# Kernel optimization log

Hardware: AMD Instinct MI355X
Metric: run time of the kernel (lower is better)

## Reference

```python
import jax, jax.numpy as jnp
import numpy as np

B, N, C, H, W = 16, 8, 3, 64, 96
PRED_BITS = 2
CONV_CH, FC, FMAP_H, FMAP_W = 16, 100, 16, 24


def _conv(x, Wc, bc):
    # x: [n, cin, 64, 96] -> [n, 16, 16, 24]; kernel 8x8, stride 4, pad 2
    y = jax.lax.conv_general_dilated(x, Wc, (4, 4), [(2, 2), (2, 2)],
                                     dimension_numbers=('NCHW', 'OIHW', 'NCHW'))
    return y + bc[None, :, None, None]


def _encoder(x, Wc, bc, W2, b2, W3, b3):
    h1 = jax.nn.relu(_conv(x, Wc, bc)).reshape(x.shape[0], -1)  # [n, 6144]
    h2 = jax.nn.relu(h1 @ W2 + b2)
    return h2 @ W3 + b3  # [n, PRED_BITS]


def _gumbel_softmax(logits, g, temp):
    return jax.nn.softmax((logits + g) / temp, axis=-1)


def setup_inputs() -> dict:
    key = jax.random.key(0)
    ks = jax.random.split(key, 16)
    rn = lambda k, s, sc=1.0: jax.random.normal(k, s, jnp.float32) * sc
    gum = lambda k, s: -jnp.log(-jnp.log(jax.random.uniform(k, s, jnp.float32, 1e-6, 1.0 - 1e-6)))
    inp = {
        'state': rn(ks[0], (B, N, C, H, W)),
        'state_next': rn(ks[1], (B, N, C, H, W)),
        'state_tilda': rn(ks[2], (B, N, C, H, W)),
        'n_obj': jax.random.randint(ks[3], (B,), 1, N + 1),
        'temp': jnp.asarray(1.0, jnp.float32),
        'g_unary': gum(ks[4], (3, B * N, PRED_BITS)),
        'g_binary': gum(ks[5], (3, B * N * N, PRED_BITS)),
        'Wc_u': rn(ks[6], (CONV_CH, C, 8, 8), 0.05),
        'bc_u': jnp.zeros((CONV_CH,), jnp.float32),
        'W2_u': rn(ks[7], (CONV_CH * FMAP_H * FMAP_W, FC), 0.02),
        'b2_u': jnp.zeros((FC,), jnp.float32),
        'W3_u': rn(ks[8], (FC, PRED_BITS), 0.1),
        'b3_u': jnp.zeros((PRED_BITS,), jnp.float32),
        'Wc_b': rn(ks[9], (CONV_CH, 2 * C, 8, 8), 0.05),
        'bc_b': jnp.zeros((CONV_CH,), jnp.float32),
        'W2_b': rn(ks[10], (CONV_CH * FMAP_H * FMAP_W, FC), 0.02),
        'b2_b': jnp.zeros((FC,), jnp.float32),
        'W3_b': rn(ks[11], (FC, PRED_BITS), 0.1),
        'b3_b': jnp.zeros((PRED_BITS,), jnp.float32),
    }
    return inp


def reference(state, state_next, state_tilda, n_obj, temp, g_unary, g_binary,
              Wc_u, bc_u, W2_u, b2_u, W3_u, b3_u,
              Wc_b, bc_b, W2_b, b2_b, W3_b, b3_b):
    # cartesian-product pair gather (padded to N_max^2 per sample)
    ii = jnp.arange(N * N) // N
    jj = jnp.arange(N * N) % N

    def pairs(s):  # [B,N,C,H,W] -> [B*N*N, 2C, H, W]
        return jnp.concatenate([s[:, ii], s[:, jj]], axis=2).reshape(B * N * N, 2 * C, H, W)

    def bin_pred(s, g):
        logits = _encoder(pairs(s), Wc_b, bc_b, W2_b, b2_b, W3_b, b3_b)
        return _gumbel_softmax(logits, g, temp).reshape(B, N * N, PRED_BITS)

    def un_pred(s, g):
        logits = _encoder(s.reshape(B * N, C, H, W), Wc_u, bc_u, W2_u, b2_u, W3_u, b3_u)
        return _gumbel_softmax(logits, g, temp).reshape(B, N, PRED_BITS)

    bp = bin_pred(state, g_binary[0])
    bp_n = bin_pred(state_next, g_binary[1])
    bp_t = bin_pred(state_tilda, g_binary[2])
    up = un_pred(state, g_unary[0])
    up_n = un_pred(state_next, g_unary[1])
    up_t = un_pred(state_tilda, g_unary[2])

    # compact the valid n^2 pairs to the front (matches torch padded scatter layout)
    n = n_obj[:, None]                      # [B,1]
    p = jnp.arange(N * N)[None, :]          # [1,N^2]
    ns = jnp.maximum(n, 1)
    k = (p // ns) * N + (p % ns)            # padded index of compact position p
    valid_b = (p < n * n)[:, :, None]
    kidx = jnp.clip(k, 0, N * N - 1)[:, :, None]

    def compact(x):
        return jnp.take_along_axis(x, kidx, axis=1) * valid_b

    valid_u = (jnp.arange(N)[None, :] < n)[:, :, None]

    return (compact(bp), compact(bp_n), compact(bp_t),
            up * valid_u, up_n * valid_u, up_t * valid_u)
```

## Files before the change

### kernel.cpp

```cpp
#include <hip/hip_runtime.h>
#include <hip/hip_fp16.h>


typedef __attribute__((ext_vector_type(8))) _Float16 f16x8;
typedef __attribute__((ext_vector_type(4))) float f32x4;

__device__ inline unsigned short h16u(float x) {
    __half h = __float2half(x);
    return __builtin_bit_cast(unsigned short, h);
}

__device__ inline uint4 pair_relu4(uint4 f, uint4 s) {
    f16x8 a = __builtin_bit_cast(f16x8, f);
    f16x8 b = __builtin_bit_cast(f16x8, s);
    const f16x8 z = {0, 0, 0, 0, 0, 0, 0, 0};
    f16x8 r = a + b;
    r = __builtin_elementwise_max(r, z);
    return __builtin_bit_cast(uint4, r);
}

#define CL_STRIDE 106
#define CL_CH (36 * CL_STRIDE)
__global__ __launch_bounds__(256) void conv_prep_kernel(
    const float* __restrict__ s0, const float* __restrict__ s1, const float* __restrict__ s2,
    const float* __restrict__ Wcu, const float* __restrict__ Wcb,
    const float* __restrict__ bcu, const float* __restrict__ bcb,
    const float* __restrict__ W2b, const float* __restrict__ W2u,
    unsigned short* __restrict__ Au, unsigned short* __restrict__ yfb,
    unsigned short* __restrict__ ysb,
    unsigned short* __restrict__ Btb, unsigned short* __restrict__ Btu)
{
    __shared__ __align__(16) unsigned short sh[3 * CL_CH];
    const int bx  = blockIdx.x;
    const int tid = threadIdx.x;

    if (bx >= 768) {
        const int bx2 = bx - 768;
        const int arr = bx2 / 48;
        const int k0 = (bx2 % 48) * 128;
        const float* W2 = arr ? W2u : W2b;
        unsigned short* Bt = arr ? Btu : Btb;
#pragma unroll
        for (int p = 0; p < 2; ++p) {
            const int kk0 = p * 64;
            __syncthreads();
            for (int t = tid; t < 64 * 128; t += 256) {
                int kk = t >> 7, f = t & 127;
                float v = (f < 100) ? W2[(long)(k0 + kk0 + kk) * 100 + f] : 0.f;
                sh[kk * 130 + f] = h16u(v);
            }
            __syncthreads();
            for (int t = tid; t < 64 * 128; t += 256) {
                int f = t >> 6, kk = t & 63;
                Bt[(long)f * 6144 + k0 + kk0 + kk] = sh[kk * 130 + f];
            }
        }
        return;
    }

    const int si  = bx >> 8;
    const int rem = bx & 255;
    const int img = rem >> 1;
    const int h   = rem & 1;
    const float* simg = (si == 0 ? s0 : (si == 1 ? s1 : s2)) + (long)img * 18432;

    const int lane = tid & 63;
    const int w    = tid >> 6;
    const int quad = lane >> 4;
    const int lcol = lane & 15;

    {
        unsigned* d = (unsigned*)sh;
        const float4* Wu4 = (const float4*)Wcu;
        for (int l4 = tid; l4 < 768; l4 += 256) {
            int l = l4 * 4, ch = l / 192, e = l % 192;
            int g = (e >> 5) * 3;
            int bi = ((g * 64 + ((e >> 3) & 3) * 16 + ch) * 8 + (e & 7)) >> 1;
            float4 v = Wu4[l4];
            d[bi]     = (unsigned)h16u(v.x) | ((unsigned)h16u(v.y) << 16);
            d[bi + 1] = (unsigned)h16u(v.z) | ((unsigned)h16u(v.w) << 16);
        }
        const float4* Wb4 = (const float4*)Wcb;
        for (int l4 = tid; l4 < 1536; l4 += 256) {
            int l = l4 * 4, ch = l / 384, r = l % 384;
            int nt = (r < 192) ? 1 : 2, e = r % 192;
            int g = (e >> 5) * 3 + nt;
            int bi = ((g * 64 + ((e >> 3) & 3) * 16 + ch) * 8 + (e & 7)) >> 1;
            float4 v = Wb4[l4];
            d[bi]     = (unsigned)h16u(v.x) | ((unsigned)h16u(v.y) << 16);
            d[bi + 1] = (unsigned)h16u(v.z) | ((unsigned)h16u(v.w) << 16);
        }
    }
    __syncthreads();

    f16x8 bw[6][3];
#pragma unroll
    for (int t6 = 0; t6 < 6; ++t6)
#pragma unroll
        for (int nt = 0; nt < 3; ++nt)
            bw[t6][nt] = *(const f16x8*)(sh + ((t6 * 3 + nt) * 64 + lane) * 8);
    __syncthreads();

    for (int t = tid; t < (3 * CL_CH) / 2; t += 256)
        ((unsigned*)sh)[t] = 0u;
    __syncthreads();

    const int y0 = h * 32;
    for (int t = tid; t < 3 * 36 * 24; t += 256) {
        int c = t / 864, rq = t % 864, r = rq / 24, q = rq % 24;
        int iy = y0 + r - 2;
        if (iy >= 0 && iy < 64) {
            float4 v = *((const float4*)(simg + c * 6144 + iy * 96) + q);
            unsigned lo = (unsigned)h16u(v.x) | ((unsigned)h16u(v.y) << 16);
            unsigned hi = (unsigned)h16u(v.z) | ((unsigned)h16u(v.w) << 16);
            unsigned* dst = (unsigned*)(sh + c * CL_CH + r * CL_STRIDE + q * 4 + 4);
            dst[0] = lo; dst[1] = hi;
        }
    }
    __syncthreads();

    const float bu = bcu[lcol];
    const float bb = bcb[lcol];

    f32x4 accs[3][3];
#pragma unroll
    for (int mi = 0; mi < 3; ++mi)
#pragma unroll
        for (int nt = 0; nt < 3; ++nt) accs[mi][nt] = (f32x4){0.f, 0.f, 0.f, 0.f};

#pragma unroll
    for (int mi = 0; mi < 3; ++mi) {
        const int mt = w * 3 + mi;
        const int p  = mt * 16 + lcol;
        const int oyl = p / 24, ox = p % 24;
#pragma unroll
        for (int t6 = 0; t6 < 6; ++t6) {
            int g  = t6 * 4 + quad;
            int c  = g >> 3, ky = g & 7;
            const unsigned* lp = (const unsigned*)(sh + c * CL_CH + (oyl * 4 + ky) * CL_STRIDE + ox * 4 + 2);
            f16x8 afr;
            unsigned* ap = (unsigned*)&afr;
            ap[0] = lp[0]; ap[1] = lp[1]; ap[2] = lp[2]; ap[3] = lp[3];
            accs[mi][0] = __builtin_amdgcn_mfma_f32_16x16x32_f16(afr, bw[t6][0], accs[mi][0], 0, 0, 0);
            accs[mi][1] = __builtin_amdgcn_mfma_f32_16x16x32_f16(afr, bw[t6][1], accs[mi][1], 0, 0, 0);
            accs[mi][2] = __builtin_amdgcn_mfma_f32_16x16x32_f16(afr, bw[t6][2], accs[mi][2], 0, 0, 0);
        }
    }
    __syncthreads();

#pragma unroll
    for (int mi = 0; mi < 3; ++mi) {
        const int base = (w * 3 + mi) * 16 + quad * 4;
#pragma unroll
        for (int nt = 0; nt < 3; ++nt) {
            ushort4 o;
#pragma unroll
            for (int reg = 0; reg < 4; ++reg) {
                float v = accs[mi][nt][reg];
                if (nt == 0) { v += bu; v = v > 0.f ? v : 0.f; }
                else if (nt == 1) v += bb;
                ((unsigned short*)&o)[reg] = h16u(v);
            }
            *(ushort4*)(sh + (nt * 16 + lcol) * 200 + base) = o;
        }
    }
    __syncthreads();

    const long im = (long)si * 128 + img;
    unsigned short* outp[3] = { Au + im * 6144, yfb + im * 6144, ysb + im * 6144 };
    for (int t = tid; t < 1152; t += 256) {
        int nt = t / 384, r = t % 384, ch = r / 24, q = r % 24;
        uint4 v = *(const uint4*)(sh + (nt * 16 + ch) * 200 + q * 8);
        *(uint4*)(outp[nt] + ch * 384 + h * 192 + q * 8) = v;
    }
}

__global__ __launch_bounds__(256) void gemm_kernel(
    const unsigned short* __restrict__ yfb, const unsigned short* __restrict__ ysb,
    const unsigned short* __restrict__ Au,
    const unsigned short* __restrict__ Btb, const unsigned short* __restrict__ Btu,
    __half* __restrict__ partial)
{
    const int tid = threadIdx.x;
    const int mt = blockIdx.x % 54;
    const int kc = blockIdx.x / 54;

    __shared__ __align__(16) unsigned short lsA[64 * 72];
    __shared__ __align__(16) unsigned short lsB[128 * 72];

    const int lane = tid & 63;
    const int w  = tid >> 6;
    const int wr = w & 1;
    const int wc = w >> 1;
    const int quad = lane >> 4;
    const int lcol = lane & 15;

    f32x4 acc[2][4];
#pragma unroll
    for (int i = 0; i < 2; ++i)
#pragma unroll
        for (int j = 0; j < 4; ++j) acc[i][j] = (f32x4){0.f, 0.f, 0.f, 0.f};

    const int ra = tid >> 2, qa = tid & 3;
    const bool fused = (mt < 48);
    const unsigned short *pf, *ps = nullptr;
    if (fused) {
        int g = mt * 64 + ra;
        int si = g >> 10, gs = g & 1023;
        int b = gs >> 6, i = (gs >> 3) & 7, j = gs & 7;
        pf = yfb + (long)(si * 128 + b * 8 + i) * 6144;
        ps = ysb + (long)(si * 128 + b * 8 + j) * 6144;
    } else {
        pf = Au + (long)((mt - 48) * 64 + ra) * 6144;
    }
    const unsigned short* Bt = fused ? Btb : Btu;
    const int rb = tid >> 1, hb = tid & 1;
    const long brow = (long)rb * 6144;
    const int kbase0 = kc * 768;

    for (int it = 0; it < 12; ++it) {
        const int kb = kbase0 + it * 64;
        const uint4* gb = (const uint4*)(Bt + brow + kb + hb * 32);
        uint4 b0 = gb[0], b1 = gb[1], b2 = gb[2], b3 = gb[3];
        const uint4* gf = (const uint4*)(pf + kb + qa * 16);
        uint4 f0 = gf[0], f1 = gf[1];
        if (fused) {
            const uint4* gs2 = (const uint4*)(ps + kb + qa * 16);
            f0 = pair_relu4(f0, gs2[0]);
            f1 = pair_relu4(f1, gs2[1]);
        }
        uint4* da = (uint4*)(lsA + ra * 72 + qa * 16);
        uint4* db = (uint4*)(lsB + rb * 72 + hb * 32);
        da[0] = f0; da[1] = f1;
        db[0] = b0; db[1] = b1; db[2] = b2; db[3] = b3;
        __syncthreads();
#pragma unroll
        for (int ks = 0; ks < 2; ++ks) {
            f16x8 af[2], bfr[4];
#pragma unroll
            for (int t = 0; t < 2; ++t)
                af[t] = *(const f16x8*)(lsA + (wr * 32 + t * 16 + lcol) * 72 + ks * 32 + quad * 8);
#pragma unroll
            for (int t = 0; t < 4; ++t)
                bfr[t] = *(const f16x8*)(lsB + (wc * 64 + t * 16 + lcol) * 72 + ks * 32 + quad * 8);
#pragma unroll
            for (int i = 0; i < 2; ++i)
#pragma unroll
                for (int j = 0; j < 4; ++j)
                    acc[i][j] = __builtin_amdgcn_mfma_f32_16x16x32_f16(af[i], bfr[j], acc[i][j], 0, 0, 0);
        }
        __syncthreads();
    }

    __half* out = partial + (long)(kc * 54 + mt) * 8192;
#pragma unroll
    for (int i = 0; i < 2; ++i)
#pragma unroll
        for (int j = 0; j < 4; ++j)
#pragma unroll
            for (int reg = 0; reg < 4; ++reg) {
                int rr = wr * 32 + i * 16 + quad * 4 + reg;
                int cc = wc * 64 + j * 16 + lcol;
                out[rr * 128 + cc] = __float2half(acc[i][j][reg]);
            }
}

__global__ __launch_bounds__(256) void head_kernel(
    const __half* __restrict__ partial,
    const float* __restrict__ b2b, const float* __restrict__ b2u,
    const float* __restrict__ W3b, const float* __restrict__ b3b,
    const float* __restrict__ W3u, const float* __restrict__ b3u,
    const float* __restrict__ gb, const float* __restrict__ gu,
    const int* __restrict__ nobj, const float* __restrict__ temp_p,
    float* __restrict__ out)
{
    const int tid = threadIdx.x;
    const int dp = blockIdx.x * 16 + (tid >> 4);
    const int c = tid & 15;
    const bool un = dp >= 3072;

    int srcrow, validf;
    long gidx, oidx;
    if (!un) {
        int si = dp / 1024, rem = dp % 1024;
        int b = rem >> 6, p = rem & 63;
        int n = nobj[b];
        int ns = n > 0 ? n : 1;
        int k = (p / ns) * 8 + (p % ns);
        validf = p < n * n;
        int kk = k < 63 ? k : 63;
        srcrow = si * 1024 + b * 64 + kk;
        gidx = (long)srcrow * 2;
        oidx = (long)si * 2048 + (b * 64 + p) * 2;
    } else {
        int r = dp - 3072;
        int si = r / 128, q = r % 128;
        int b = q >> 3, i = q & 7;
        srcrow = 3072 + r;
        validf = i < nobj[b];
        gidx = (long)si * 256 + q * 2;
        oidx = 6144 + (long)si * 256 + q * 2;
    }

    const float* b2 = un ? b2u : b2b;
    const float* W3 = un ? W3u : W3b;
    const int mt = srcrow >> 6, rr = srcrow & 63;
    float l0 = 0.f, l1 = 0.f;
    for (int f = c; f < 100; f += 16) {
        float s = b2[f];
#pragma unroll
        for (int kc = 0; kc < 8; ++kc)
            s += __half2float(partial[((long)(kc * 54 + mt) * 64 + rr) * 128 + f]);
        float hv = s > 0.f ? s : 0.f;
        l0 = fmaf(hv, W3[f * 2],     l0);
        l1 = fmaf(hv, W3[f * 2 + 1], l1);
    }
#pragma unroll
    for (int off = 8; off >= 1; off >>= 1) {
        l0 += __shfl_xor(l0, off);
        l1 += __shfl_xor(l1, off);
    }
    if (c == 0) {
        const float* b3 = un ? b3u : b3b;
        const float* g = (un ? gu : gb) + gidx;
        float d = ((l0 + b3[0] + g[0]) - (l1 + b3[1] + g[1])) / temp_p[0];
        float p0 = 1.f / (1.f + expf(-d));
        out[oidx]     = validf ? p0 : 0.f;
        out[oidx + 1] = validf ? 1.f - p0 : 0.f;
    }
}

static const size_t YFB_OFF  = 0;
static const size_t YSB_OFF  = 4718592;
static const size_t AU_OFF   = 9437184;
static const size_t BTB_OFF  = 14155776;
static const size_t BTU_OFF  = 15728640;
static const size_t PART_OFF = 17301504;

extern "C" void kernel_launch(void* const* d_in, const int* in_sizes, int n_in,
                              void* d_out, int out_size, void* d_ws, size_t ws_size,
                              hipStream_t stream) {
    const float* state   = (const float*)d_in[0];
    const float* state_n = (const float*)d_in[1];
    const float* state_t = (const float*)d_in[2];
    const int*   n_obj   = (const int*)  d_in[3];
    const float* temp    = (const float*)d_in[4];
    const float* g_un    = (const float*)d_in[5];
    const float* g_bin   = (const float*)d_in[6];
    const float* Wc_u    = (const float*)d_in[7];
    const float* bc_u    = (const float*)d_in[8];
    const float* W2_u    = (const float*)d_in[9];
    const float* b2_u    = (const float*)d_in[10];
    const float* W3_u    = (const float*)d_in[11];
    const float* b3_u    = (const float*)d_in[12];
    const float* Wc_b    = (const float*)d_in[13];
    const float* bc_b    = (const float*)d_in[14];
    const float* W2_b    = (const float*)d_in[15];
    const float* b2_b    = (const float*)d_in[16];
    const float* W3_b    = (const float*)d_in[17];
    const float* b3_b    = (const float*)d_in[18];

    char* ws = (char*)d_ws;
    unsigned short* yfb  = (unsigned short*)(ws + YFB_OFF);
    unsigned short* ysb  = (unsigned short*)(ws + YSB_OFF);
    unsigned short* Au   = (unsigned short*)(ws + AU_OFF);
    unsigned short* Btb  = (unsigned short*)(ws + BTB_OFF);
    unsigned short* Btu  = (unsigned short*)(ws + BTU_OFF);
    __half*         prt  = (__half*)(ws + PART_OFF);
    float*          out  = (float*)d_out;

    hipLaunchKernelGGL(conv_prep_kernel, dim3(864), dim3(256), 0, stream,
                       state, state_n, state_t, Wc_u, Wc_b, bc_u, bc_b, W2_b, W2_u,
                       Au, yfb, ysb, Btb, Btu);
    hipLaunchKernelGGL(gemm_kernel, dim3(432), dim3(256), 0, stream,
                       yfb, ysb, Au, Btb, Btu, prt);
    hipLaunchKernelGGL(head_kernel, dim3(216), dim3(256), 0, stream,
                       prt, b2_b, b2_u, W3_b, b3_b, W3_u, b3_u,
                       g_bin, g_un, n_obj, temp, out);
}
```

Before: 150.4 us.

## Fuse conv, GEMM and head into one cooperative persistent kernel with grid syncs

Replaces the three kernel launches with a single cooperative launch of 256 blocks. Each block loops over the conv/prep items and the GEMM tiles, and grid-wide syncs separate the phases before the head runs. This is meant to remove launch gaps and inter-kernel tail idle time. The cost is less parallelism per phase: 864 conv items and 432 GEMM tiles become multiple waves on 256 blocks, and each grid sync adds its own overhead. The GEMM loop moves its barrier to before the shared-memory stores, and the old three-kernel path is kept as a fallback if the cooperative launch fails.

After: 331.2 us. 120% more time.

```diff
diff --git a/kernel.cpp b/kernel.cpp
--- a/kernel.cpp
+++ b/kernel.cpp
@@ -1,5 +1,8 @@
 #include <hip/hip_runtime.h>
 #include <hip/hip_fp16.h>
+#include <hip/hip_cooperative_groups.h>
+
+namespace cg = cooperative_groups;
 
 
 typedef __attribute__((ext_vector_type(8))) _Float16 f16x8;
@@ -21,21 +24,19 @@
 
 #define CL_STRIDE 106
 #define CL_CH (36 * CL_STRIDE)
-__global__ __launch_bounds__(256) void conv_prep_kernel(
-    const float* __restrict__ s0, const float* __restrict__ s1, const float* __restrict__ s2,
-    const float* __restrict__ Wcu, const float* __restrict__ Wcb,
-    const float* __restrict__ bcu, const float* __restrict__ bcb,
-    const float* __restrict__ W2b, const float* __restrict__ W2u,
-    unsigned short* __restrict__ Au, unsigned short* __restrict__ yfb,
-    unsigned short* __restrict__ ysb,
-    unsigned short* __restrict__ Btb, unsigned short* __restrict__ Btu)
-{
-    __shared__ __align__(16) unsigned short sh[3 * CL_CH];
-    const int bx  = blockIdx.x;
-    const int tid = threadIdx.x;
-
-    if (bx >= 768) {
-        const int bx2 = bx - 768;
+#define SH_SHORTS 13824
+
+__device__ void conv_item(
+    int item, int tid, unsigned short* sh,
+    const float* s0, const float* s1, const float* s2,
+    const float* Wcu, const float* Wcb,
+    const float* bcu, const float* bcb,
+    const float* W2b, const float* W2u,
+    unsigned short* Au, unsigned short* yfb, unsigned short* ysb,
+    unsigned short* Btb, unsigned short* Btu)
+{
+    if (item >= 768) {
+        const int bx2 = item - 768;
         const int arr = bx2 / 48;
         const int k0 = (bx2 % 48) * 128;
         const float* W2 = arr ? W2u : W2b;
@@ -58,8 +59,8 @@
         return;
     }
 
-    const int si  = bx >> 8;
-    const int rem = bx & 255;
+    const int si  = item >> 8;
+    const int rem = item & 255;
     const int img = rem >> 1;
     const int h   = rem & 1;
     const float* simg = (si == 0 ? s0 : (si == 1 ? s1 : s2)) + (long)img * 18432;
@@ -167,26 +168,28 @@
     __syncthreads();
 
     const long im = (long)si * 128 + img;
-    unsigned short* outp[3] = { Au + im * 6144, yfb + im * 6144, ysb + im * 6144 };
+    unsigned short* outp0 = Au  + im * 6144;
+    unsigned short* outp1 = yfb + im * 6144;
+    unsigned short* outp2 = ysb + im * 6144;
     for (int t = tid; t < 1152; t += 256) {
         int nt = t / 384, r = t % 384, ch = r / 24, q = r % 24;
         uint4 v = *(const uint4*)(sh + (nt * 16 + ch) * 200 + q * 8);
-        *(uint4*)(outp[nt] + ch * 384 + h * 192 + q * 8) = v;
-    }
-}
-
-__global__ __launch_bounds__(256) void gemm_kernel(
-    const unsigned short* __restrict__ yfb, const unsigned short* __restrict__ ysb,
-    const unsigned short* __restrict__ Au,
-    const unsigned short* __restrict__ Btb, const unsigned short* __restrict__ Btu,
-    __half* __restrict__ partial)
-{
-    const int tid = threadIdx.x;
-    const int mt = blockIdx.x % 54;
-    const int kc = blockIdx.x / 54;
-
-    __shared__ __align__(16) unsigned short lsA[64 * 72];
-    __shared__ __align__(16) unsigned short lsB[128 * 72];
+        unsigned short* op = (nt == 0) ? outp0 : (nt == 1) ? outp1 : outp2;
+        *(uint4*)(op + ch * 384 + h * 192 + q * 8) = v;
+    }
+}
+
+__device__ void gemm_tile(
+    int tile, int tid, unsigned short* sh,
+    const unsigned short* yfb, const unsigned short* ysb,
+    const unsigned short* Au,
+    const unsigned short* Btb, const unsigned short* Btu,
+    __half* partial)
+{
+    unsigned short* lsA = sh;
+    unsigned short* lsB = sh + 64 * 72;
+    const int mt = tile % 54;
+    const int kc = tile / 54;
 
     const int lane = tid & 63;
     const int w  = tid >> 6;
@@ -220,8 +223,8 @@
 
     for (int it = 0; it < 12; ++it) {
         const int kb = kbase0 + it * 64;
-        const uint4* gb = (const uint4*)(Bt + brow + kb + hb * 32);
-        uint4 b0 = gb[0], b1 = gb[1], b2 = gb[2], b3 = gb[3];
+        const uint4* gbp = (const uint4*)(Bt + brow + kb + hb * 32);
+        uint4 b0 = gbp[0], b1 = gbp[1], b2 = gbp[2], b3 = gbp[3];
         const uint4* gf = (const uint4*)(pf + kb + qa * 16);
         uint4 f0 = gf[0], f1 = gf[1];
         if (fused) {
@@ -229,6 +232,7 @@
             f0 = pair_relu4(f0, gs2[0]);
             f1 = pair_relu4(f1, gs2[1]);
         }
+        __syncthreads();
         uint4* da = (uint4*)(lsA + ra * 72 + qa * 16);
         uint4* db = (uint4*)(lsB + rb * 72 + hb * 32);
         da[0] = f0; da[1] = f1;
@@ -249,10 +253,9 @@
                 for (int j = 0; j < 4; ++j)
                     acc[i][j] = __builtin_amdgcn_mfma_f32_16x16x32_f16(af[i], bfr[j], acc[i][j], 0, 0, 0);
         }
-        __syncthreads();
-    }
-
-    __half* out = partial + (long)(kc * 54 + mt) * 8192;
+    }
+
+    __half* op = partial + (long)(kc * 54 + mt) * 8192;
 #pragma unroll
     for (int i = 0; i < 2; ++i)
 #pragma unroll
@@ -261,24 +264,21 @@
             for (int reg = 0; reg < 4; ++reg) {
                 int rr = wr * 32 + i * 16 + quad * 4 + reg;
                 int cc = wc * 64 + j * 16 + lcol;
-                out[rr * 128 + cc] = __float2half(acc[i][j][reg]);
+                op[rr * 128 + cc] = __float2half(acc[i][j][reg]);
             }
 }
 
-__global__ __launch_bounds__(256) void head_kernel(
-    const __half* __restrict__ partial,
-    const float* __restrict__ b2b, const float* __restrict__ b2u,
-    const float* __restrict__ W3b, const float* __restrict__ b3b,
-    const float* __restrict__ W3u, const float* __restrict__ b3u,
-    const float* __restrict__ gb, const float* __restrict__ gu,
-    const int* __restrict__ nobj, const float* __restrict__ temp_p,
-    float* __restrict__ out)
-{
-    const int tid = threadIdx.x;
-    const int dp = blockIdx.x * 16 + (tid >> 4);
-    const int c = tid & 15;
+__device__ void head_task(
+    int dp, int c,
+    const __half* partial,
+    const float* b2b, const float* b2u,
+    const float* W3b, const float* b3b,
+    const float* W3u, const float* b3u,
+    const float* gb, const float* gu,
+    const int* nobj, const float* temp_p,
+    float* out)
+{
     const bool un = dp >= 3072;
-
     int srcrow, validf;
     long gidx, oidx;
     if (!un) {
@@ -304,13 +304,13 @@
 
     const float* b2 = un ? b2u : b2b;
     const float* W3 = un ? W3u : W3b;
-    const int mt = srcrow >> 6, rr = srcrow & 63;
+    const int mt2 = srcrow >> 6, rr = srcrow & 63;
     float l0 = 0.f, l1 = 0.f;
     for (int f = c; f < 100; f += 16) {
         float s = b2[f];
 #pragma unroll
-        for (int kc = 0; kc < 8; ++kc)
-            s += __half2float(partial[((long)(kc * 54 + mt) * 64 + rr) * 128 + f]);
+        for (int kc2 = 0; kc2 < 8; ++kc2)
+            s += __half2float(partial[((long)(kc2 * 54 + mt2) * 64 + rr) * 128 + f]);
         float hv = s > 0.f ? s : 0.f;
         l0 = fmaf(hv, W3[f * 2],     l0);
         l1 = fmaf(hv, W3[f * 2 + 1], l1);
@@ -328,6 +328,88 @@
         out[oidx]     = validf ? p0 : 0.f;
         out[oidx + 1] = validf ? 1.f - p0 : 0.f;
     }
+}
+
+__global__ __launch_bounds__(256) void fused_all(
+    const float* s0, const float* s1, const float* s2,
+    const float* Wcu, const float* Wcb,
+    const float* bcu, const float* bcb,
+    const float* W2b, const float* W2u,
+    unsigned short* Au, unsigned short* yfb, unsigned short* ysb,
+    unsigned short* Btb, unsigned short* Btu,
+    __half* partial,
+    const float* b2b, const float* b2u,
+    const float* W3b, const float* b3b,
+    const float* W3u, const float* b3u,
+    const float* gb, const float* gu,
+    const int* nobj, const float* temp_p,
+    float* out)
+{
+    __shared__ __align__(16) unsigned short sh[SH_SHORTS];
+    const int bx  = blockIdx.x;
+    const int tid = threadIdx.x;
+    cg::grid_group grid = cg::this_grid();
+
+    for (int item = bx; item < 864; item += 256) {
+        conv_item(item, tid, sh, s0, s1, s2, Wcu, Wcb, bcu, bcb, W2b, W2u,
+                  Au, yfb, ysb, Btb, Btu);
+        __syncthreads();
+    }
+
+    __threadfence();
+    grid.sync();
+
+    for (int t = bx; t < 432; t += 256)
+        gemm_tile(t, tid, sh, yfb, ysb, Au, Btb, Btu, partial);
+
+    __threadfence();
+    grid.sync();
+
+    {
+        const int dp = bx * 16 + (tid >> 4);
+        if (dp < 3456)
+            head_task(dp, tid & 15, partial, b2b, b2u, W3b, b3b, W3u, b3u,
+                      gb, gu, nobj, temp_p, out);
+    }
+}
+
+__global__ __launch_bounds__(256) void conv_sep(
+    const float* __restrict__ s0, const float* __restrict__ s1, const float* __restrict__ s2,
+    const float* __restrict__ Wcu, const float* __restrict__ Wcb,
+    const float* __restrict__ bcu, const float* __restrict__ bcb,
+    const float* __restrict__ W2b, const float* __restrict__ W2u,
+    unsigned short* __restrict__ Au, unsigned short* __restrict__ yfb,
+    unsigned short* __restrict__ ysb,
+    unsigned short* __restrict__ Btb, unsigned short* __restrict__ Btu)
+{
+    __shared__ __align__(16) unsigned short sh[SH_SHORTS];
+    conv_item(blockIdx.x, threadIdx.x, sh, s0, s1, s2, Wcu, Wcb, bcu, bcb,
+              W2b, W2u, Au, yfb, ysb, Btb, Btu);
+}
+
+__global__ __launch_bounds__(256) void gemm_sep(
+    const unsigned short* __restrict__ yfb, const unsigned short* __restrict__ ysb,
+    const unsigned short* __restrict__ Au,
+    const unsigned short* __restrict__ Btb, const unsigned short* __restrict__ Btu,
+    __half* __restrict__ partial)
+{
+    __shared__ __align__(16) unsigned short sh[SH_SHORTS];
+    gemm_tile(blockIdx.x, threadIdx.x, sh, yfb, ysb, Au, Btb, Btu, partial);
+}
+
+__global__ __launch_bounds__(256) void head_sep(
+    const __half* __restrict__ partial,
+    const float* __restrict__ b2b, const float* __restrict__ b2u,
+    const float* __restrict__ W3b, const float* __restrict__ b3b,
+    const float* __restrict__ W3u, const float* __restrict__ b3u,
+    const float* __restrict__ gb, const float* __restrict__ gu,
+    const int* __restrict__ nobj, const float* __restrict__ temp_p,
+    float* __restrict__ out)
+{
+    const int dp = blockIdx.x * 16 + (threadIdx.x >> 4);
+    if (dp < 3456)
+        head_task(dp, threadIdx.x & 15, partial, b2b, b2u, W3b, b3b, W3u, b3u,
+                  gb, gu, nobj, temp_p, out);
 }
 
 static const size_t YFB_OFF  = 0;
@@ -369,12 +451,31 @@
     __half*         prt  = (__half*)(ws + PART_OFF);
     float*          out  = (float*)d_out;
 
-    hipLaunchKernelGGL(conv_prep_kernel, dim3(864), dim3(256), 0, stream,
-                       state, state_n, state_t, Wc_u, Wc_b, bc_u, bc_b, W2_b, W2_u,
-                       Au, yfb, ysb, Btb, Btu);
-    hipLaunchKernelGGL(gemm_kernel, dim3(432), dim3(256), 0, stream,
-                       yfb, ysb, Au, Btb, Btu, prt);
-    hipLaunchKernelGGL(head_kernel, dim3(216), dim3(256), 0, stream,
-                       prt, b2_b, b2_u, W3_b, b3_b, W3_u, b3_u,
-                       g_bin, g_un, n_obj, temp, out);
-}
+    void* args[] = {
+        (void*)&state, (void*)&state_n, (void*)&state_t,
+        (void*)&Wc_u, (void*)&Wc_b, (void*)&bc_u, (void*)&bc_b,
+        (void*)&W2_b, (void*)&W2_u,
+        (void*)&Au, (void*)&yfb, (void*)&ysb,
+        (void*)&Btb, (void*)&Btu,
+        (void*)&prt,
+        (void*)&b2_b, (void*)&b2_u,
+        (void*)&W3_b, (void*)&b3_b,
+        (void*)&W3_u, (void*)&b3_u,
+        (void*)&g_bin, (void*)&g_un,
+        (void*)&n_obj, (void*)&temp,
+        (void*)&out
+    };
+    hipError_t err = hipLaunchCooperativeKernel((const void*)fused_all,
+                                                dim3(256), dim3(256),
+                                                args, 0, stream);
+    if (err != hipSuccess) {
+        hipLaunchKernelGGL(conv_sep, dim3(864), dim3(256), 0, stream,
+                           state, state_n, state_t, Wc_u, Wc_b, bc_u, bc_b,
+                           W2_b, W2_u, Au, yfb, ysb, Btb, Btu);
+        hipLaunchKernelGGL(gemm_sep, dim3(432), dim3(256), 0, stream,
+                           yfb, ysb, Au, Btb, Btu, prt);
+        hipLaunchKernelGGL(head_sep, dim3(216), dim3(256), 0, stream,
+                           prt, b2_b, b2_u, W3_b, b3_b, W3_u, b3_u,
+                           g_bin, g_un, n_obj, temp, out);
+    }
+}
```
